# Optimization experiments

Measured on AMD Instinct MI355X. Metric: run time of the kernel, lower is better.

Reference implementation:

```python
import jax, jax.numpy as jnp
import numpy as np

NUM_HEADS = 16


def setup_inputs() -> dict:
    key = jax.random.key(0)
    ks = jax.random.split(key, 5)
    B, S, D = 2, 2048, 2048
    scale = 1.0 / np.sqrt(D)
    return {
        "x": jax.random.normal(ks[0], (B, S, D), dtype=jnp.float32),
        "W_q": jax.random.normal(ks[1], (D, D), dtype=jnp.float32) * scale,
        "W_k": jax.random.normal(ks[2], (D, D), dtype=jnp.float32) * scale,
        "W_v": jax.random.normal(ks[3], (D, D), dtype=jnp.float32) * scale,
        "W_o": jax.random.normal(ks[4], (D, D), dtype=jnp.float32) * scale,
        "b_o": jnp.zeros((D,), dtype=jnp.float32),
    }


def reference(x, W_q, W_k, W_v, W_o, b_o):
    B, S, D = x.shape
    H = NUM_HEADS
    hd = D // H
    # projections, split into heads: [B, H, S, hd]
    q = (x @ W_q).reshape(B, S, H, hd).transpose(0, 2, 1, 3)
    k = (x @ W_k).reshape(B, S, H, hd).transpose(0, 2, 1, 3)
    v = (x @ W_v).reshape(B, S, H, hd).transpose(0, 2, 1, 3)
    # causal attention with explicit score matrix [B, H, S, S]
    scores = jnp.einsum("bhqd,bhkd->bhqk", q, k) / jnp.sqrt(jnp.asarray(hd, x.dtype))
    causal = jnp.tril(jnp.ones((S, S), dtype=bool))  # True = keep
    scores = jnp.where(causal, scores, -jnp.inf)
    weights = jax.nn.softmax(scores, axis=-1)
    ctx = jnp.einsum("bhqk,bhkd->bhqd", weights, v)
    ctx = ctx.transpose(0, 2, 1, 3).reshape(B, S, D)
    return ctx @ W_o + b_o
```

## Files before the change

kernel.cpp:

```cpp
#include <hip/hip_runtime.h>
#include <stdint.h>

#define SQ_S 2048
#define DIM 2048
#define NH 16
#define HD 128
#define NB 2
#define NROWS (NB * SQ_S)
#define NQKV (3 * DIM)
#define NQK (2 * DIM)

typedef __bf16 bf16x8 __attribute__((ext_vector_type(8)));
typedef float f32x4 __attribute__((ext_vector_type(4)));
typedef float f32x16 __attribute__((ext_vector_type(16)));
typedef unsigned short u16;

__device__ __forceinline__ u16 f2bf(float f) {
    unsigned int u = __float_as_uint(f);
    u += 0x7FFF + ((u >> 16) & 1);
    return (u16)(u >> 16);
}

__device__ __forceinline__ void load_lds16(const u16* g, u16* lds) {
    __builtin_amdgcn_global_load_lds(
        (const __attribute__((address_space(1))) unsigned int*)(uintptr_t)g,
        (__attribute__((address_space(3))) unsigned int*)(unsigned int)(uintptr_t)lds,
        16, 0, 0);
}

__global__ __launch_bounds__(256) void cast_x_kernel(const float* __restrict__ in,
                                                     u16* __restrict__ out) {
    int i = (blockIdx.x * 256 + threadIdx.x) * 4;
    float4 v = *(const float4*)(in + i);
    ushort4 o;
    o.x = f2bf(v.x); o.y = f2bf(v.y); o.z = f2bf(v.z); o.w = f2bf(v.w);
    *(ushort4*)(out + i) = o;
}

__global__ __launch_bounds__(256) void transpose_w_kernel(
    const float* __restrict__ w0, const float* __restrict__ w1,
    const float* __restrict__ w2, const float* __restrict__ w3,
    u16* __restrict__ o0, u16* __restrict__ o1,
    u16* __restrict__ o2, u16* __restrict__ o3) {
    __shared__ u16 tile[64][65];
    int z = blockIdx.z;
    const float* in = z == 0 ? w0 : z == 1 ? w1 : z == 2 ? w2 : w3;
    u16* out = z == 0 ? o0 : z == 1 ? o1 : z == 2 ? o2 : o3;
    int r0 = blockIdx.y * 64, c0 = blockIdx.x * 64;
    int t = threadIdx.x;
#pragma unroll
    for (int i = 0; i < 16; ++i) {
        int idx = i * 256 + t;
        int r = idx >> 6, c = idx & 63;
        tile[r][c] = f2bf(in[(size_t)(r0 + r) * DIM + c0 + c]);
    }
    __syncthreads();
#pragma unroll
    for (int i = 0; i < 4; ++i) {
        int idx = i * 256 + t;
        int oc = idx >> 4;
        int r4 = (idx & 15) * 4;
        ushort4 v;
        v.x = tile[r4 + 0][oc]; v.y = tile[r4 + 1][oc];
        v.z = tile[r4 + 2][oc]; v.w = tile[r4 + 3][oc];
        *(ushort4*)(out + (size_t)(c0 + oc) * DIM + r0 + r4) = v;
    }
}

__global__ __launch_bounds__(256) void gemm_qkv(const u16* __restrict__ A,
                                                const u16* __restrict__ Bt,
                                                u16* __restrict__ QKo,
                                                u16* __restrict__ Vt) {
    __shared__ u16 As[128 * 64];
    __shared__ u16 Bs[128 * 64];
    const int K = DIM;
    int t = threadIdx.x;
    int w = t >> 6, l = t & 63;
    int wm = (w >> 1) * 64, wn = (w & 1) * 64;
    int m32 = l & 31, kh = l >> 5;
    int bm = blockIdx.y, bn = blockIdx.x;
    int st_gcol = (((t & 7) ^ ((t >> 3) & 7)) * 8);
    f32x16 acc[2][2] = {};

    for (int k0 = 0; k0 < K; k0 += 64) {
        __syncthreads();
#pragma unroll
        for (int c = 0; c < 4; ++c) {
            int e = c * 2048 + t * 8;
            int row = e >> 6;
            load_lds16(A + (size_t)(bm * 128 + row) * K + k0 + st_gcol, As + e);
        }
#pragma unroll
        for (int c = 0; c < 4; ++c) {
            int e = c * 2048 + t * 8;
            int row = e >> 6;
            load_lds16(Bt + (size_t)(bn * 128 + row) * K + k0 + st_gcol, Bs + e);
        }
        __syncthreads();
#pragma unroll
        for (int ks = 0; ks < 4; ++ks) {
            bf16x8 a[2], b[2];
#pragma unroll
            for (int mt = 0; mt < 2; ++mt)
                a[mt] = *(const bf16x8*)(As + (wm + mt * 32 + m32) * 64 +
                                         (((ks * 2 + kh) ^ (m32 & 7)) * 8));
#pragma unroll
            for (int nt = 0; nt < 2; ++nt)
                b[nt] = *(const bf16x8*)(Bs + (wn + nt * 32 + m32) * 64 +
                                         (((ks * 2 + kh) ^ (m32 & 7)) * 8));
#pragma unroll
            for (int mt = 0; mt < 2; ++mt)
#pragma unroll
                for (int nt = 0; nt < 2; ++nt)
                    acc[mt][nt] = __builtin_amdgcn_mfma_f32_32x32x16_bf16(a[mt], b[nt], acc[mt][nt], 0, 0, 0);
        }
    }
    int r0 = bm * 128 + wm, c0 = bn * 128 + wn;
    if (bn < 32) {
#pragma unroll
        for (int mt = 0; mt < 2; ++mt)
#pragma unroll
            for (int nt = 0; nt < 2; ++nt) {
                int col = c0 + nt * 32 + m32;
#pragma unroll
                for (int i = 0; i < 16; ++i) {
                    int row = r0 + mt * 32 + (i & 3) + 8 * (i >> 2) + 4 * kh;
                    QKo[(size_t)row * NQK + col] = f2bf(acc[mt][nt][i]);
                }
            }
    } else {
#pragma unroll
        for (int mt = 0; mt < 2; ++mt)
#pragma unroll
            for (int nt = 0; nt < 2; ++nt) {
                int colv = c0 + nt * 32 + m32 - 4096;
                int h = colv >> 7, dd = colv & 127;
#pragma unroll
                for (int g = 0; g < 4; ++g) {
                    int row = r0 + mt * 32 + 8 * g + 4 * kh;
                    int b = row >> 11, s = row & 2047;
                    ushort4 v4;
                    v4.x = f2bf(acc[mt][nt][g * 4 + 0]);
                    v4.y = f2bf(acc[mt][nt][g * 4 + 1]);
                    v4.z = f2bf(acc[mt][nt][g * 4 + 2]);
                    v4.w = f2bf(acc[mt][nt][g * 4 + 3]);
                    *(ushort4*)(Vt + (((size_t)(b * NH + h) * HD + dd) * SQ_S + s)) = v4;
                }
            }
    }
}

__global__ __launch_bounds__(256) void gemm_out(const u16* __restrict__ A,
                                                const u16* __restrict__ Bt,
                                                float* __restrict__ C,
                                                const float* __restrict__ bias) {
    __shared__ u16 As[128 * 64];
    __shared__ u16 Bs[128 * 64];
    const int K = DIM, N = DIM;
    int t = threadIdx.x;
    int w = t >> 6, l = t & 63;
    int wm = (w >> 1) * 64, wn = (w & 1) * 64;
    int m32 = l & 31, kh = l >> 5;
    int bm = blockIdx.y, bn = blockIdx.x;
    int st_gcol = (((t & 7) ^ ((t >> 3) & 7)) * 8);
    f32x16 acc[2][2] = {};

    for (int k0 = 0; k0 < K; k0 += 64) {
        __syncthreads();
#pragma unroll
        for (int c = 0; c < 4; ++c) {
            int e = c * 2048 + t * 8;
            int row = e >> 6;
            load_lds16(A + (size_t)(bm * 128 + row) * K + k0 + st_gcol, As + e);
        }
#pragma unroll
        for (int c = 0; c < 4; ++c) {
            int e = c * 2048 + t * 8;
            int row = e >> 6;
            load_lds16(Bt + (size_t)(bn * 128 + row) * K + k0 + st_gcol, Bs + e);
        }
        __syncthreads();
#pragma unroll
        for (int ks = 0; ks < 4; ++ks) {
            bf16x8 a[2], b[2];
#pragma unroll
            for (int mt = 0; mt < 2; ++mt)
                a[mt] = *(const bf16x8*)(As + (wm + mt * 32 + m32) * 64 +
                                         (((ks * 2 + kh) ^ (m32 & 7)) * 8));
#pragma unroll
            for (int nt = 0; nt < 2; ++nt)
                b[nt] = *(const bf16x8*)(Bs + (wn + nt * 32 + m32) * 64 +
                                         (((ks * 2 + kh) ^ (m32 & 7)) * 8));
#pragma unroll
            for (int mt = 0; mt < 2; ++mt)
#pragma unroll
                for (int nt = 0; nt < 2; ++nt)
                    acc[mt][nt] = __builtin_amdgcn_mfma_f32_32x32x16_bf16(a[mt], b[nt], acc[mt][nt], 0, 0, 0);
        }
    }
    int r0 = bm * 128 + wm, c0 = bn * 128 + wn;
#pragma unroll
    for (int mt = 0; mt < 2; ++mt)
#pragma unroll
        for (int nt = 0; nt < 2; ++nt) {
            int col = c0 + nt * 32 + m32;
            float bb = bias[col];
#pragma unroll
            for (int i = 0; i < 16; ++i) {
                int row = r0 + mt * 32 + (i & 3) + 8 * (i >> 2) + 4 * kh;
                C[(size_t)row * N + col] = acc[mt][nt][i] + bb;
            }
        }
}

__global__ __launch_bounds__(256) void attn_kernel(const u16* __restrict__ Q,
                                                   const u16* __restrict__ K,
                                                   const u16* __restrict__ Vt,
                                                   u16* __restrict__ ctx, int ldqk) {
    __shared__ u16 Kl[2][64 * 128];
    __shared__ u16 Vl[2][128 * 64];
    __shared__ u16 Pl[4][16 * 64];
    int t = threadIdx.x;
    int w = t >> 6, l = t & 63;
    int lr = l & 15, q = l >> 4, lk = q * 8;
    int bid = blockIdx.x;
    int r_  = bid >> 3;
    int px  = r_ & 15;
    int h   = (bid & 7) + ((r_ >> 4) & 1) * 8;
    int b   = r_ >> 5;
    const float scale = 0.08838834764831845f;
    int stK_gcol = (((t & 15) ^ (t >> 4)) * 8);
    int stV_gcol = (((t & 7) ^ ((t >> 3) & 7)) * 8);
    const u16* Kbase = K + (size_t)b * SQ_S * ldqk + h * HD;
    const u16* Vbase = Vt + ((size_t)(b * NH + h)) * HD * SQ_S;

#pragma unroll 1
    for (int pass = 0; pass < 2; ++pass) {
        int qt = pass == 0 ? px : 31 - px;
        int q0 = qt * 64;
        int njt = qt + 1;

        bf16x8 qf[4];
        {
            const u16* qp = Q + ((size_t)(b * SQ_S + q0 + w * 16 + lr)) * ldqk + h * HD;
#pragma unroll
            for (int kd = 0; kd < 4; ++kd)
                qf[kd] = *(const bf16x8*)(qp + kd * 32 + lk);
        }

        f32x4 o[8] = {};
        float l_r[4] = {0.f, 0.f, 0.f, 0.f};

        {
            int e = t * 8;
#pragma unroll
            for (int c = 0; c < 4; ++c) {
                int eK = c * 2048 + e;
                load_lds16(Kbase + (size_t)(eK >> 7) * ldqk + stK_gcol, Kl[0] + eK);
            }
#pragma unroll
            for (int c = 0; c < 4; ++c) {
                int eV = c * 2048 + e;
                load_lds16(Vbase + (size_t)(eV >> 6) * SQ_S + stV_gcol, Vl[0] + eV);
            }
        }

#pragma unroll 1
        for (int jt = 0; jt < njt; ++jt) {
            __syncthreads();
            if (jt + 1 < njt) {
                int j1 = (jt + 1) * 64;
                u16* Kd = Kl[(jt + 1) & 1];
                u16* Vd = Vl[(jt + 1) & 1];
                int e = t * 8;
#pragma unroll
                for (int c = 0; c < 4; ++c) {
                    int eK = c * 2048 + e;
                    load_lds16(Kbase + (size_t)(j1 + (eK >> 7)) * ldqk + stK_gcol, Kd + eK);
                }
#pragma unroll
                for (int c = 0; c < 4; ++c) {
                    int eV = c * 2048 + e;
                    load_lds16(Vbase + (size_t)(eV >> 6) * SQ_S + j1 + stV_gcol, Vd + eV);
                }
            }
            const u16* Kc = Kl[jt & 1];
            const u16* Vc = Vl[jt & 1];

            f32x4 s[4] = {};
#pragma unroll
            for (int kd = 0; kd < 4; ++kd) {
#pragma unroll
                for (int nt = 0; nt < 4; ++nt) {
                    bf16x8 kb = *(const bf16x8*)(Kc + (nt * 16 + lr) * 128 +
                                                 (((kd * 4 + q) ^ lr) * 8));
                    s[nt] = __builtin_amdgcn_mfma_f32_16x16x32_bf16(qf[kd], kb, s[nt], 0, 0, 0);
                }
            }
            bool diag = (jt == qt);
            float rs[4] = {0.f, 0.f, 0.f, 0.f};
            float pv[4][4];
#pragma unroll
            for (int nt = 0; nt < 4; ++nt)
#pragma unroll
                for (int r = 0; r < 4; ++r) {
                    float v = s[nt][r] * scale - 6.0f;
                    if (diag && (nt * 16 + lr > w * 16 + q * 4 + r)) v = -1.0e30f;
                    float pp = __expf(v);
                    pv[nt][r] = pp;
                    rs[r] += pp;
                }
#pragma unroll
            for (int d = 1; d < 16; d <<= 1)
#pragma unroll
                for (int r = 0; r < 4; ++r)
                    rs[r] += __shfl_xor(rs[r], d, 64);
#pragma unroll
            for (int r = 0; r < 4; ++r)
                l_r[r] += rs[r];
            u16* pw = Pl[w];
#pragma unroll
            for (int nt = 0; nt < 4; ++nt)
#pragma unroll
                for (int r = 0; r < 4; ++r) {
                    int prow = q * 4 + r;
                    int pcol = nt * 16 + lr;
                    pw[prow * 64 + (((pcol >> 3) ^ (prow & 7)) * 8) + (pcol & 7)] = f2bf(pv[nt][r]);
                }
            asm volatile("s_waitcnt lgkmcnt(0)" ::: "memory");
#pragma unroll
            for (int kj = 0; kj < 2; ++kj) {
                bf16x8 pa = *(const bf16x8*)(pw + lr * 64 + (((kj * 4 + q) ^ (lr & 7)) * 8));
#pragma unroll
                for (int nd = 0; nd < 8; ++nd) {
                    bf16x8 vb = *(const bf16x8*)(Vc + (nd * 16 + lr) * 64 +
                                                 (((kj * 4 + q) ^ (lr & 7)) * 8));
                    o[nd] = __builtin_amdgcn_mfma_f32_16x16x32_bf16(pa, vb, o[nd], 0, 0, 0);
                }
            }
        }
        float li[4];
#pragma unroll
        for (int r = 0; r < 4; ++r) li[r] = 1.f / l_r[r];
#pragma unroll
        for (int nd = 0; nd < 8; ++nd)
#pragma unroll
            for (int r = 0; r < 4; ++r) {
                int row = q0 + w * 16 + q * 4 + r;
                int col = h * HD + nd * 16 + lr;
                ctx[((size_t)(b * SQ_S + row)) * DIM + col] = f2bf(o[nd][r] * li[r]);
            }
        __syncthreads();
    }
}

extern "C" void kernel_launch(void* const* d_in, const int* in_sizes, int n_in,
                              void* d_out, int out_size, void* d_ws, size_t ws_size,
                              hipStream_t stream) {
    const float* x  = (const float*)d_in[0];
    const float* Wq = (const float*)d_in[1];
    const float* Wk = (const float*)d_in[2];
    const float* Wv = (const float*)d_in[3];
    const float* Wo = (const float*)d_in[4];
    const float* bo = (const float*)d_in[5];
    float* out = (float*)d_out;

    char* p = (char*)d_ws;
    const size_t SZ_ACT = (size_t)NROWS * DIM * 2;
    const size_t SZ_W   = (size_t)DIM * DIM * 2;
    u16* Xb   = (u16*)(p);
    u16* Wqkv = (u16*)(p + SZ_ACT);
    u16* Wot  = (u16*)(p + SZ_ACT + 3 * SZ_W);
    u16* QK   = (u16*)(p + SZ_ACT + 4 * SZ_W);
    u16* Vt   = (u16*)(p + 3 * SZ_ACT + 4 * SZ_W);
    u16* Cx   = (u16*)(p + 4 * SZ_ACT + 4 * SZ_W);

    cast_x_kernel<<<(NROWS * DIM) / 1024, 256, 0, stream>>>(x, Xb);
    transpose_w_kernel<<<dim3(DIM / 64, DIM / 64, 4), 256, 0, stream>>>(
        Wq, Wk, Wv, Wo,
        Wqkv, Wqkv + (size_t)DIM * DIM, Wqkv + 2 * (size_t)DIM * DIM, Wot);
    gemm_qkv<<<dim3(NQKV / 128, NROWS / 128), 256, 0, stream>>>(Xb, Wqkv, QK, Vt);
    attn_kernel<<<512, 256, 0, stream>>>(QK, QK + DIM, Vt, Cx, NQK);
    gemm_out<<<dim3(DIM / 128, NROWS / 128), 256, 0, stream>>>(Cx, Wot, out, bo);
}
```

Measured before the change: 369.5 us.

## Rewrite QKV and output GEMMs with 256x128 tiles and software-pipelined LDS prefetch

Replaces the two GEMM kernels with a shared core that uses 512-thread blocks on 256x128 output tiles and 16x16x32 MFMAs. It splits each 64-wide K step into two 32-wide halves, staged through a double-buffered LDS ring so global loads overlap compute. The core uses explicit waitcnt, barriers, sched_barrier and setprio around the MFMA bursts. Block IDs are remapped into a grouped order for L2 locality. The aim is to hide global-load latency and raise MFMA utilisation, at the cost of more LDS per block and hand-tuned synchronisation that is fragile.

```diff
diff --git a/kernel.cpp b/kernel.cpp
--- a/kernel.cpp
+++ b/kernel.cpp
@@ -12,7 +12,6 @@
 
 typedef __bf16 bf16x8 __attribute__((ext_vector_type(8)));
 typedef float f32x4 __attribute__((ext_vector_type(4)));
-typedef float f32x16 __attribute__((ext_vector_type(16)));
 typedef unsigned short u16;
 
 __device__ __forceinline__ u16 f2bf(float f) {
@@ -67,149 +66,182 @@
     }
 }
 
-__global__ __launch_bounds__(256) void gemm_qkv(const u16* __restrict__ A,
+#define ASZ (256 * 32)
+#define BSZ (128 * 32)
+#define NTK (DIM / 64)
+
+__device__ __forceinline__ void stage_a(const u16* __restrict__ A, int gm0, int kt, int kk,
+                                        u16* dst, int t) {
+#pragma unroll
+    for (int i = 0; i < 2; ++i) {
+        int e = (i * 512 + t) * 8;
+        int r = e >> 5;
+        int c = (t & 3) ^ (r & 3);
+        load_lds16(A + (size_t)(gm0 + r) * DIM + kt * 64 + kk * 32 + c * 8, dst + e);
+    }
+}
+__device__ __forceinline__ void stage_b(const u16* __restrict__ Bt, int gn0, int kt, int kk,
+                                        u16* dst, int t) {
+    int e = t * 8;
+    int r = e >> 5;
+    int c = (t & 3) ^ (r & 3);
+    load_lds16(Bt + (size_t)(gn0 + r) * DIM + kt * 64 + kk * 32 + c * 8, dst + e);
+}
+
+__device__ __forceinline__ bf16x8 frag(const u16* half, int row, int lq) {
+    return *(const bf16x8*)(half + row * 32 + ((lq ^ (row & 3)) * 8));
+}
+
+__device__ __forceinline__ void gemm_core(const u16* __restrict__ A, const u16* __restrict__ Bt,
+                                          int gm0, int gn0, u16* As, u16* Bs,
+                                          f32x4 acc[4][4]) {
+    int t = threadIdx.x;
+    int w = t >> 6, l = t & 63;
+    int wm = w >> 1, wn = w & 1;
+    int lr = l & 15, lq = l >> 4;
+    int ar = wm * 64 + lr;
+    int br = wn * 64 + lr;
+
+    stage_a(A, gm0, 0, 0, As + 0 * ASZ, t);
+    stage_b(Bt, gn0, 0, 0, Bs + 0 * BSZ, t);
+    stage_a(A, gm0, 0, 1, As + 1 * ASZ, t);
+    stage_b(Bt, gn0, 0, 1, Bs + 1 * BSZ, t);
+    stage_a(A, gm0, 1, 0, As + 2 * ASZ, t);
+    stage_b(Bt, gn0, 1, 0, Bs + 2 * BSZ, t);
+    asm volatile("s_waitcnt vmcnt(6)" ::: "memory");
+    __builtin_amdgcn_s_barrier();
+
+#pragma unroll 2
+    for (int kt = 0; kt < NTK; ++kt) {
+        int buf = kt & 1, nbuf = buf ^ 1;
+        const u16* a0 = As + (buf * 2 + 0) * ASZ;
+        const u16* a1 = As + (buf * 2 + 1) * ASZ;
+        const u16* b0 = Bs + (buf * 2 + 0) * BSZ;
+        const u16* b1 = Bs + (buf * 2 + 1) * BSZ;
+        bf16x8 af[4], bfr[4];
+
+#pragma unroll
+        for (int mf = 0; mf < 4; ++mf) af[mf] = frag(a0, ar + mf * 16, lq);
+#pragma unroll
+        for (int nf = 0; nf < 4; ++nf) bfr[nf] = frag(b0, br + nf * 16, lq);
+        {
+            int ks = (kt + 1 < NTK) ? kt + 1 : kt;
+            stage_a(A, gm0, ks, 1, As + (nbuf * 2 + 1) * ASZ, t);
+            stage_b(Bt, gn0, ks, 1, Bs + (nbuf * 2 + 1) * BSZ, t);
+        }
+        asm volatile("s_waitcnt vmcnt(6)" ::: "memory");
+        __builtin_amdgcn_s_barrier();
+        asm volatile("s_waitcnt lgkmcnt(0)" ::: "memory");
+        __builtin_amdgcn_sched_barrier(0);
+        __builtin_amdgcn_s_setprio(1);
+#pragma unroll
+        for (int mf = 0; mf < 4; ++mf)
+#pragma unroll
+            for (int nf = 0; nf < 4; ++nf)
+                acc[mf][nf] = __builtin_amdgcn_mfma_f32_16x16x32_bf16(af[mf], bfr[nf], acc[mf][nf], 0, 0, 0);
+        __builtin_amdgcn_s_setprio(0);
+        __builtin_amdgcn_s_barrier();
+        __builtin_amdgcn_sched_barrier(0);
+
+#pragma unroll
+        for (int mf = 0; mf < 4; ++mf) af[mf] = frag(a1, ar + mf * 16, lq);
+#pragma unroll
+        for (int nf = 0; nf < 4; ++nf) bfr[nf] = frag(b1, br + nf * 16, lq);
+        {
+            int ks = (kt + 2 < NTK) ? kt + 2 : kt;
+            stage_a(A, gm0, ks, 0, As + (buf * 2 + 0) * ASZ, t);
+            stage_b(Bt, gn0, ks, 0, Bs + (buf * 2 + 0) * BSZ, t);
+        }
+        asm volatile("s_waitcnt vmcnt(6)" ::: "memory");
+        __builtin_amdgcn_s_barrier();
+        asm volatile("s_waitcnt lgkmcnt(0)" ::: "memory");
+        __builtin_amdgcn_sched_barrier(0);
+        __builtin_amdgcn_s_setprio(1);
+#pragma unroll
+        for (int mf = 0; mf < 4; ++mf)
+#pragma unroll
+            for (int nf = 0; nf < 4; ++nf)
+                acc[mf][nf] = __builtin_amdgcn_mfma_f32_16x16x32_bf16(af[mf], bfr[nf], acc[mf][nf], 0, 0, 0);
+        __builtin_amdgcn_s_setprio(0);
+        __builtin_amdgcn_s_barrier();
+        __builtin_amdgcn_sched_barrier(0);
+    }
+    asm volatile("s_waitcnt vmcnt(0)" ::: "memory");
+}
+
+__global__ __launch_bounds__(512) void gemm_qkv(const u16* __restrict__ A,
                                                 const u16* __restrict__ Bt,
                                                 u16* __restrict__ QKo,
                                                 u16* __restrict__ Vt) {
-    __shared__ u16 As[128 * 64];
-    __shared__ u16 Bs[128 * 64];
-    const int K = DIM;
-    int t = threadIdx.x;
-    int w = t >> 6, l = t & 63;
-    int wm = (w >> 1) * 64, wn = (w & 1) * 64;
-    int m32 = l & 31, kh = l >> 5;
-    int bm = blockIdx.y, bn = blockIdx.x;
-    int st_gcol = (((t & 7) ^ ((t >> 3) & 7)) * 8);
-    f32x16 acc[2][2] = {};
-
-    for (int k0 = 0; k0 < K; k0 += 64) {
-        __syncthreads();
-#pragma unroll
-        for (int c = 0; c < 4; ++c) {
-            int e = c * 2048 + t * 8;
-            int row = e >> 6;
-            load_lds16(A + (size_t)(bm * 128 + row) * K + k0 + st_gcol, As + e);
-        }
-#pragma unroll
-        for (int c = 0; c < 4; ++c) {
-            int e = c * 2048 + t * 8;
-            int row = e >> 6;
-            load_lds16(Bt + (size_t)(bn * 128 + row) * K + k0 + st_gcol, Bs + e);
-        }
-        __syncthreads();
-#pragma unroll
-        for (int ks = 0; ks < 4; ++ks) {
-            bf16x8 a[2], b[2];
-#pragma unroll
-            for (int mt = 0; mt < 2; ++mt)
-                a[mt] = *(const bf16x8*)(As + (wm + mt * 32 + m32) * 64 +
-                                         (((ks * 2 + kh) ^ (m32 & 7)) * 8));
-#pragma unroll
-            for (int nt = 0; nt < 2; ++nt)
-                b[nt] = *(const bf16x8*)(Bs + (wn + nt * 32 + m32) * 64 +
-                                         (((ks * 2 + kh) ^ (m32 & 7)) * 8));
-#pragma unroll
-            for (int mt = 0; mt < 2; ++mt)
-#pragma unroll
-                for (int nt = 0; nt < 2; ++nt)
-                    acc[mt][nt] = __builtin_amdgcn_mfma_f32_32x32x16_bf16(a[mt], b[nt], acc[mt][nt], 0, 0, 0);
-        }
-    }
-    int r0 = bm * 128 + wm, c0 = bn * 128 + wn;
+    __shared__ u16 As[4 * ASZ];
+    __shared__ u16 Bs[4 * BSZ];
+    int bid = blockIdx.x;
+    int wg = (bid & 7) * 96 + (bid >> 3);
+    int bm = wg / 48, bn = wg % 48;
+    f32x4 acc[4][4] = {};
+    gemm_core(A, Bt, bm * 256, bn * 128, As, Bs, acc);
+
+    int t = threadIdx.x, w = t >> 6, l = t & 63;
+    int wm = w >> 1, wn = w & 1, lr = l & 15, lq = l >> 4;
+    int r0 = bm * 256 + wm * 64;
     if (bn < 32) {
-#pragma unroll
-        for (int mt = 0; mt < 2; ++mt)
-#pragma unroll
-            for (int nt = 0; nt < 2; ++nt) {
-                int col = c0 + nt * 32 + m32;
-#pragma unroll
-                for (int i = 0; i < 16; ++i) {
-                    int row = r0 + mt * 32 + (i & 3) + 8 * (i >> 2) + 4 * kh;
-                    QKo[(size_t)row * NQK + col] = f2bf(acc[mt][nt][i]);
-                }
+        int c0 = bn * 128 + wn * 64;
+#pragma unroll
+        for (int mf = 0; mf < 4; ++mf)
+#pragma unroll
+            for (int nf = 0; nf < 4; ++nf) {
+                int col = c0 + nf * 16 + lr;
+                int rowb = r0 + mf * 16 + lq * 4;
+#pragma unroll
+                for (int r = 0; r < 4; ++r)
+                    QKo[(size_t)(rowb + r) * NQK + col] = f2bf(acc[mf][nf][r]);
             }
     } else {
-#pragma unroll
-        for (int mt = 0; mt < 2; ++mt)
-#pragma unroll
-            for (int nt = 0; nt < 2; ++nt) {
-                int colv = c0 + nt * 32 + m32 - 4096;
+        int c0 = bn * 128 + wn * 64 - 4096;
+#pragma unroll
+        for (int mf = 0; mf < 4; ++mf)
+#pragma unroll
+            for (int nf = 0; nf < 4; ++nf) {
+                int colv = c0 + nf * 16 + lr;
                 int h = colv >> 7, dd = colv & 127;
-#pragma unroll
-                for (int g = 0; g < 4; ++g) {
-                    int row = r0 + mt * 32 + 8 * g + 4 * kh;
-                    int b = row >> 11, s = row & 2047;
-                    ushort4 v4;
-                    v4.x = f2bf(acc[mt][nt][g * 4 + 0]);
-                    v4.y = f2bf(acc[mt][nt][g * 4 + 1]);
-                    v4.z = f2bf(acc[mt][nt][g * 4 + 2]);
-                    v4.w = f2bf(acc[mt][nt][g * 4 + 3]);
-                    *(ushort4*)(Vt + (((size_t)(b * NH + h) * HD + dd) * SQ_S + s)) = v4;
-                }
-            }
-    }
-}
-
-__global__ __launch_bounds__(256) void gemm_out(const u16* __restrict__ A,
+                int rowb = r0 + mf * 16 + lq * 4;
+                int b = rowb >> 11, s = rowb & 2047;
+                ushort4 v4;
+                v4.x = f2bf(acc[mf][nf][0]);
+                v4.y = f2bf(acc[mf][nf][1]);
+                v4.z = f2bf(acc[mf][nf][2]);
+                v4.w = f2bf(acc[mf][nf][3]);
+                *(ushort4*)(Vt + (((size_t)(b * NH + h) * HD + dd) * SQ_S + s)) = v4;
+            }
+    }
+}
+
+__global__ __launch_bounds__(512) void gemm_out(const u16* __restrict__ A,
                                                 const u16* __restrict__ Bt,
                                                 float* __restrict__ C,
                                                 const float* __restrict__ bias) {
-    __shared__ u16 As[128 * 64];
-    __shared__ u16 Bs[128 * 64];
-    const int K = DIM, N = DIM;
-    int t = threadIdx.x;
-    int w = t >> 6, l = t & 63;
-    int wm = (w >> 1) * 64, wn = (w & 1) * 64;
-    int m32 = l & 31, kh = l >> 5;
-    int bm = blockIdx.y, bn = blockIdx.x;
-    int st_gcol = (((t & 7) ^ ((t >> 3) & 7)) * 8);
-    f32x16 acc[2][2] = {};
-
-    for (int k0 = 0; k0 < K; k0 += 64) {
-        __syncthreads();
-#pragma unroll
-        for (int c = 0; c < 4; ++c) {
-            int e = c * 2048 + t * 8;
-            int row = e >> 6;
-            load_lds16(A + (size_t)(bm * 128 + row) * K + k0 + st_gcol, As + e);
-        }
-#pragma unroll
-        for (int c = 0; c < 4; ++c) {
-            int e = c * 2048 + t * 8;
-            int row = e >> 6;
-            load_lds16(Bt + (size_t)(bn * 128 + row) * K + k0 + st_gcol, Bs + e);
-        }
-        __syncthreads();
-#pragma unroll
-        for (int ks = 0; ks < 4; ++ks) {
-            bf16x8 a[2], b[2];
-#pragma unroll
-            for (int mt = 0; mt < 2; ++mt)
-                a[mt] = *(const bf16x8*)(As + (wm + mt * 32 + m32) * 64 +
-                                         (((ks * 2 + kh) ^ (m32 & 7)) * 8));
-#pragma unroll
-            for (int nt = 0; nt < 2; ++nt)
-                b[nt] = *(const bf16x8*)(Bs + (wn + nt * 32 + m32) * 64 +
-                                         (((ks * 2 + kh) ^ (m32 & 7)) * 8));
-#pragma unroll
-            for (int mt = 0; mt < 2; ++mt)
-#pragma unroll
-                for (int nt = 0; nt < 2; ++nt)
-                    acc[mt][nt] = __builtin_amdgcn_mfma_f32_32x32x16_bf16(a[mt], b[nt], acc[mt][nt], 0, 0, 0);
-        }
-    }
-    int r0 = bm * 128 + wm, c0 = bn * 128 + wn;
-#pragma unroll
-    for (int mt = 0; mt < 2; ++mt)
-#pragma unroll
-        for (int nt = 0; nt < 2; ++nt) {
-            int col = c0 + nt * 32 + m32;
+    __shared__ u16 As[4 * ASZ];
+    __shared__ u16 Bs[4 * BSZ];
+    int bid = blockIdx.x;
+    int wg = (bid & 7) * 32 + (bid >> 3);
+    int bm = wg >> 4, bn = wg & 15;
+    f32x4 acc[4][4] = {};
+    gemm_core(A, Bt, bm * 256, bn * 128, As, Bs, acc);
+
+    int t = threadIdx.x, w = t >> 6, l = t & 63;
+    int wm = w >> 1, wn = w & 1, lr = l & 15, lq = l >> 4;
+    int r0 = bm * 256 + wm * 64;
+    int c0 = bn * 128 + wn * 64;
+#pragma unroll
+    for (int mf = 0; mf < 4; ++mf)
+#pragma unroll
+        for (int nf = 0; nf < 4; ++nf) {
+            int col = c0 + nf * 16 + lr;
             float bb = bias[col];
-#pragma unroll
-            for (int i = 0; i < 16; ++i) {
-                int row = r0 + mt * 32 + (i & 3) + 8 * (i >> 2) + 4 * kh;
-                C[(size_t)row * N + col] = acc[mt][nt][i] + bb;
-            }
+            int rowb = r0 + mf * 16 + lq * 4;
+#pragma unroll
+            for (int r = 0; r < 4; ++r)
+                C[(size_t)(rowb + r) * DIM + col] = acc[mf][nf][r] + bb;
         }
 }
 
@@ -379,7 +411,7 @@
     transpose_w_kernel<<<dim3(DIM / 64, DIM / 64, 4), 256, 0, stream>>>(
         Wq, Wk, Wv, Wo,
         Wqkv, Wqkv + (size_t)DIM * DIM, Wqkv + 2 * (size_t)DIM * DIM, Wot);
-    gemm_qkv<<<dim3(NQKV / 128, NROWS / 128), 256, 0, stream>>>(Xb, Wqkv, QK, Vt);
+    gemm_qkv<<<768, 512, 0, stream>>>(Xb, Wqkv, QK, Vt);
     attn_kernel<<<512, 256, 0, stream>>>(QK, QK + DIM, Vt, Cx, NQK);
-    gemm_out<<<dim3(DIM / 128, NROWS / 128), 256, 0, stream>>>(Cx, Wot, out, bo);
-}
+    gemm_out<<<256, 512, 0, stream>>>(Cx, Wot, out, bo);
+}
```

After: 367.4 us. No clear change (-0.6%).
